# Kernel optimization log

Hardware: AMD Instinct MI355X
Metric: run time of the kernel (lower is better)

Reference implementation:

```python
import jax, jax.numpy as jnp
import numpy as np

K = 16          # number of nearest neighbors (kernel_size)
BN_EPS = 1e-5   # BatchNorm eps
LRELU_SLOPE = 0.2


def setup_inputs() -> dict:
    key = jax.random.key(0)
    k1, k2 = jax.random.split(key)
    B, C, N = 2, 64, 8192
    C_out = 64
    x = jax.random.normal(k1, (B, C, N, 1), dtype=jnp.float32)
    # Conv2d(in_channels*2, out_channels, kernel_size=1, bias=False)
    W = jax.random.normal(k2, (C_out, 2 * C), dtype=jnp.float32) * (1.0 / np.sqrt(2 * C))
    gamma = jnp.ones((C_out,), dtype=jnp.float32)
    beta = jnp.zeros((C_out,), dtype=jnp.float32)
    return {"x": x, "W": W, "gamma": gamma, "beta": beta}


def _knn_idx(f):
    """f: (B, C, N) point features. Returns nn_idx (B, N, K) of nearest neighbors
    (by squared euclidean distance, including self)."""
    pts = jnp.transpose(f, (0, 2, 1))                     # (B, N, C)
    sq = jnp.sum(pts * pts, axis=-1)                      # (B, N)
    inner = jnp.einsum('bnc,bmc->bnm', pts, pts)          # (B, N, N)
    dist = sq[:, :, None] - 2.0 * inner + sq[:, None, :]  # (B, N, N) squared dist
    # torch.topk(-pairwise_distance, k) -> indices of k smallest distances
    _, nn_idx = jax.lax.top_k(-dist, K)                   # (B, N, K)
    return nn_idx


def reference(x, W, gamma, beta):
    # x: (B, C, N, 1)
    f = x[:, :, :, 0]                                     # (B, C, N)
    nn_idx = _knn_idx(jax.lax.stop_gradient(f))           # (B, N, K), no grad (torch.no_grad)

    # EdgeConv features: x_i = center (broadcast), x_j = gathered neighbors
    x_j = jax.vmap(lambda fb, ib: fb[:, ib])(f, nn_idx)   # (B, C, N, K)
    x_i = f[:, :, :, None]                                # (B, C, N, 1) broadcasts over K
    feat = jnp.concatenate(
        [jnp.broadcast_to(x_i, x_j.shape), x_j - x_i], axis=1)  # (B, 2C, N, K)

    # 1x1 conv (no bias)
    y = jnp.einsum('oc,bcnk->bonk', W, feat)              # (B, C_out, N, K)

    # BatchNorm2d (training mode: batch statistics, biased variance)
    mean = jnp.mean(y, axis=(0, 2, 3), keepdims=True)
    var = jnp.mean(jnp.square(y - mean), axis=(0, 2, 3), keepdims=True)
    y = (y - mean) * jax.lax.rsqrt(var + BN_EPS)
    y = y * gamma[None, :, None, None] + beta[None, :, None, None]

    # LeakyReLU(0.2)
    y = jnp.where(y >= 0, y, LRELU_SLOPE * y)

    # max over neighbors
    return jnp.max(y, axis=-1)                            # (B, C_out, N)
```

## Files before the change

kernel.cpp:

```cpp
#include <hip/hip_runtime.h>
#include <hip/hip_bf16.h>

#define B 2
#define C 64
#define N 8192
#define K 16
#define CO 64
#define KSEG 4
#define NSTEP (N / KSEG / 64)

using s8v    = __attribute__((ext_vector_type(8)))  short;
using f32x16 = __attribute__((ext_vector_type(16))) float;

__device__ __forceinline__ unsigned short f2bf(float f) {
    unsigned u = __builtin_bit_cast(unsigned, f);
    u += 0x7fffu + ((u >> 16) & 1u);
    return (unsigned short)(u >> 16);
}
__device__ __forceinline__ float bf2f(unsigned short h) {
    unsigned u = ((unsigned)h) << 16;
    return __builtin_bit_cast(float, u);
}
__device__ __forceinline__ void gl_lds16(const void* g, void* l) {
    __builtin_amdgcn_global_load_lds((const __attribute__((address_space(1))) unsigned int*)g,
                                     (__attribute__((address_space(3))) unsigned int*)l, 16, 0, 0);
}

__global__ __launch_bounds__(256) void k_sqnorm(const float* __restrict__ f,
                                                float* __restrict__ sq) {
    int i = blockIdx.x * 256 + threadIdx.x;
    int b = i >> 13;
    int n = i & (N - 1);
    const float* fp = f + (size_t)b * C * N + n;
    float s = 0.f;
#pragma unroll
    for (int c = 0; c < C; ++c) {
        float v = fp[(size_t)c * N];
        s += v * v;
    }
    sq[i] = s;
}

__global__ __launch_bounds__(256) void k_prep(const float* __restrict__ x,
                                              unsigned short* __restrict__ Xh,
                                              unsigned short* __restrict__ Xm,
                                              unsigned short* __restrict__ Xl) {
    __shared__ float lt[64][65];
    int bid = blockIdx.x;
    int b = bid >> 7;
    int n0 = (bid & 127) * 64;
    int tid = threadIdx.x;
    int quarter = tid >> 6, j = tid & 63;
#pragma unroll
    for (int cc = 0; cc < 16; ++cc) {
        int c = quarter * 16 + cc;
        lt[c][j] = x[((size_t)b * C + c) * N + n0 + j];
    }
    __syncthreads();
#pragma unroll
    for (int cc = 0; cc < 16; ++cc) {
        int nl = quarter * 16 + cc;
        float v = lt[j][nl];
        unsigned short h = f2bf(v);
        float r1 = v - bf2f(h);
        unsigned short m = f2bf(r1);
        unsigned short l = f2bf(r1 - bf2f(m));
        size_t row = ((size_t)b * N + n0 + nl) * 64 + j;
        Xh[row] = h; Xm[row] = m; Xl[row] = l;
    }
}

__global__ __launch_bounds__(256, 2) void k_knn(
        const unsigned short* __restrict__ Xh,
        const unsigned short* __restrict__ Xm,
        const unsigned short* __restrict__ Xl,
        const float* __restrict__ sq,
        float* __restrict__ partd, int* __restrict__ parti) {
    __shared__ __align__(16) unsigned short lds[2][3][64 * 64];

    int bid = blockIdx.x;
    int seg = bid & 3;
    int qb  = (bid >> 2) & 63;
    int b   = bid >> 8;
    int tid = threadIdx.x;
    int w = tid >> 6, lane = tid & 63;
    int l31 = lane & 31, lhi = lane >> 5;
    int q = qb * 128 + w * 32 + l31;

    const unsigned short* Xs[3] = {Xh, Xm, Xl};

    s8v qf[3][4];
    {
        size_t qrow = ((size_t)b * N + q) * 64;
#pragma unroll
        for (int s = 0; s < 3; ++s)
#pragma unroll
            for (int kt = 0; kt < 4; ++kt)
                qf[s][kt] = *(const s8v*)&Xs[s][qrow + kt * 16 + lhi * 8];
    }

    float bd[16];
    int   bi16[16];
#pragma unroll
    for (int j = 0; j < 16; ++j) { bd[j] = -3.4e38f; bi16[j] = -1; }
    float worst = -3.4e38f;
    int wslot = 0;

    int segbase = seg * (N / KSEG);
    int srcRowOff = lane >> 3;
    int srcChunk  = (lane & 7) ^ (lane >> 3);

    {
        int cand0 = segbase;
#pragma unroll
        for (int jj = 0; jj < 6; ++jj) {
            int is = w * 6 + jj;
            int split = is >> 3, r0 = (is & 7) * 8;
            const unsigned short* gsrc = Xs[split] +
                ((size_t)(b * N + cand0 + r0 + srcRowOff)) * 64 + srcChunk * 8;
            gl_lds16(gsrc, &lds[0][split][r0 * 64]);
        }
    }

    for (int t = 0; t < NSTEP; ++t) {
        int cand0 = segbase + t * 64;
        int cb = t & 1;

        f32x16 acc[2];
#pragma unroll
        for (int ct = 0; ct < 2; ++ct) {
#pragma unroll
            for (int g = 0; g < 4; ++g) {
                float4 sv = *(const float4*)&sq[b * N + cand0 + ct * 32 + g * 8 + 4 * lhi];
                acc[ct][g * 4 + 0] = -0.5f * sv.x;
                acc[ct][g * 4 + 1] = -0.5f * sv.y;
                acc[ct][g * 4 + 2] = -0.5f * sv.z;
                acc[ct][g * 4 + 3] = -0.5f * sv.w;
            }
        }
        asm volatile("" ::: "memory");

        if (t + 1 < NSTEP) {
            int cn = cand0 + 64;
#pragma unroll
            for (int jj = 0; jj < 6; ++jj) {
                int is = w * 6 + jj;
                int split = is >> 3, r0 = (is & 7) * 8;
                const unsigned short* gsrc = Xs[split] +
                    ((size_t)(b * N + cn + r0 + srcRowOff)) * 64 + srcChunk * 8;
                gl_lds16(gsrc, &lds[cb ^ 1][split][r0 * 64]);
            }
            asm volatile("s_waitcnt vmcnt(6)" ::: "memory");
        } else {
            asm volatile("s_waitcnt vmcnt(0)" ::: "memory");
        }
        __syncthreads();

#pragma unroll
        for (int ct = 0; ct < 2; ++ct) {
            int arow = ct * 32 + l31;
            s8v af[3][4];
#pragma unroll
            for (int s = 0; s < 3; ++s)
#pragma unroll
                for (int kt = 0; kt < 4; ++kt)
                    af[s][kt] = *(const s8v*)&lds[cb][s][arow * 64 + (((kt * 2 + lhi) ^ (arow & 7)) * 8)];
            f32x16 a = acc[ct];
#pragma unroll
            for (int kt = 0; kt < 4; ++kt) {
                a = __builtin_amdgcn_mfma_f32_32x32x16_bf16(af[1][kt], qf[1][kt], a, 0, 0, 0);
                a = __builtin_amdgcn_mfma_f32_32x32x16_bf16(af[0][kt], qf[2][kt], a, 0, 0, 0);
                a = __builtin_amdgcn_mfma_f32_32x32x16_bf16(af[2][kt], qf[0][kt], a, 0, 0, 0);
                a = __builtin_amdgcn_mfma_f32_32x32x16_bf16(af[0][kt], qf[1][kt], a, 0, 0, 0);
                a = __builtin_amdgcn_mfma_f32_32x32x16_bf16(af[1][kt], qf[0][kt], a, 0, 0, 0);
                a = __builtin_amdgcn_mfma_f32_32x32x16_bf16(af[0][kt], qf[0][kt], a, 0, 0, 0);
            }
#pragma unroll
            for (int r = 0; r < 16; ++r) {
                float sc = a[r];
                if (sc > worst) {
                    int idx = cand0 + ct * 32 + (r & 3) + 8 * (r >> 2) + 4 * lhi;
#pragma unroll
                    for (int j = 0; j < 16; ++j)
                        if (j == wslot) { bd[j] = sc; bi16[j] = idx; }
                    worst = bd[0]; wslot = 0;
#pragma unroll
                    for (int j = 1; j < 16; ++j)
                        if (bd[j] < worst) { worst = bd[j]; wslot = j; }
                }
            }
        }
        __syncthreads();
    }

    int listid = seg * 2 + lhi;
    int bq = b * N + q;
#pragma unroll
    for (int j = 0; j < 16; ++j) {
        partd[(listid * 16 + j) * (B * N) + bq] = -bd[j];
        parti[(listid * 16 + j) * (B * N) + bq] = bi16[j];
    }
}

__global__ __launch_bounds__(256) void k_merge(const float* __restrict__ partd,
                                               const int* __restrict__ parti,
                                               int* __restrict__ nn) {
    int i = blockIdx.x * 256 + threadIdx.x;
    float bd[16];
    int   bi16[16];
#pragma unroll
    for (int j = 0; j < 16; ++j) { bd[j] = 3.4e38f; bi16[j] = -1; }
    float worst = 3.4e38f;
    int wslot = 0;
    for (int t = 0; t < 8 * 16; ++t) {
        float key = partd[t * (B * N) + i];
        int   idx = parti[t * (B * N) + i];
        if (key < worst) {
#pragma unroll
            for (int j = 0; j < 16; ++j)
                if (j == wslot) { bd[j] = key; bi16[j] = idx; }
            worst = bd[0]; wslot = 0;
#pragma unroll
            for (int j = 1; j < 16; ++j)
                if (bd[j] > worst) { worst = bd[j]; wslot = j; }
        }
    }
#pragma unroll
    for (int j = 0; j < 16; ++j) nn[i * 16 + j] = bi16[j];
}

__global__ __launch_bounds__(256) void k_ag(const float* __restrict__ f,
                                            const float* __restrict__ W,
                                            float* __restrict__ A,
                                            float* __restrict__ G) {
    __shared__ float lw[CO * 129];
    __shared__ float lf[C * 64];
    int bid = blockIdx.x;
    int b = bid >> 7;
    int n0 = (bid & 127) * 64;
    int tid = threadIdx.x;

    for (int idx = tid; idx < CO * 128; idx += 256) {
        int o = idx >> 7, c = idx & 127;
        lw[o * 129 + c] = W[idx];
    }
    for (int idx = tid; idx < C * 64; idx += 256) {
        int c = idx >> 6, nl = idx & 63;
        lf[idx] = f[(size_t)b * C * N + (size_t)c * N + n0 + nl];
    }
    __syncthreads();

    int o = tid & 63, qq = tid >> 6;
    for (int ii = 0; ii < 16; ++ii) {
        int nl = qq * 16 + ii;
        float fa = 0.f, fg = 0.f;
#pragma unroll
        for (int c = 0; c < C; ++c) {
            float fv = lf[c * 64 + nl];
            fa += lw[o * 129 + c] * fv;
            fg += lw[o * 129 + 64 + c] * fv;
        }
        int n = n0 + nl;
        A[((size_t)b * N + n) * 64 + o] = fa;
        G[((size_t)b * N + n) * 64 + o] = fg;
    }
}

__global__ __launch_bounds__(256) void k_stats(const float* __restrict__ A,
                                               const float* __restrict__ G,
                                               const int* __restrict__ nn,
                                               float* __restrict__ ymax,
                                               float* __restrict__ ymin,
                                               float* __restrict__ stats) {
    __shared__ int lidx[64 * K];
    __shared__ float red[256];
    int bid = blockIdx.x;
    int b = bid >> 7;
    int n0 = (bid & 127) * 64;
    int tid = threadIdx.x;

    for (int idx = tid; idx < 64 * K; idx += 256)
        lidx[idx] = nn[((size_t)b * N + n0) * K + idx];
    __syncthreads();

    int o = tid & 63, qq = tid >> 6;
    const float* Gb = G + (size_t)b * N * 64;
    float ssum = 0.f, ssq = 0.f;
    for (int ii = 0; ii < 16; ++ii) {
        int nl = qq * 16 + ii;
        int n = n0 + nl;
        float a = A[((size_t)b * N + n) * 64 + o];
        float g = Gb[(size_t)n * 64 + o];
        float d = a - g;
        float s1 = 0.f, s2 = 0.f;
        float gmx = -3.4e38f, gmn = 3.4e38f;
#pragma unroll
        for (int k = 0; k < K; ++k) {
            int j = lidx[nl * K + k];
            float gj = Gb[(size_t)j * 64 + o];
            s1 += gj;
            s2 += gj * gj;
            gmx = fmaxf(gmx, gj);
            gmn = fminf(gmn, gj);
        }
        ymax[((size_t)b * N + n) * 64 + o] = d + gmx;
        ymin[((size_t)b * N + n) * 64 + o] = d + gmn;
        ssum += (float)K * d + s1;
        ssq  += (float)K * d * d + 2.f * d * s1 + s2;
    }

    red[tid] = ssum; __syncthreads();
    if (qq == 0) {
        float t = red[o] + red[64 + o] + red[128 + o] + red[192 + o];
        atomicAdd(&stats[o], t);
    }
    __syncthreads();
    red[tid] = ssq; __syncthreads();
    if (qq == 0) {
        float t = red[o] + red[64 + o] + red[128 + o] + red[192 + o];
        atomicAdd(&stats[64 + o], t);
    }
}

__global__ __launch_bounds__(256) void k_final(const float* __restrict__ ymax,
                                               const float* __restrict__ ymin,
                                               const float* __restrict__ stats,
                                               const float* __restrict__ gamma,
                                               const float* __restrict__ beta,
                                               float* __restrict__ out) {
    __shared__ float lt[64 * 65];
    int bid = blockIdx.x;
    int b = bid >> 7;
    int n0 = (bid & 127) * 64;
    int tid = threadIdx.x;
    int o = tid & 63, qq = tid >> 6;

    const float Mcnt = (float)(B * N * K);
    float s1 = stats[o], s2 = stats[64 + o];
    float mean = s1 / Mcnt;
    float var = s2 / Mcnt - mean * mean;
    float inv = rsqrtf(var + 1e-5f);
    float scale = gamma[o] * inv;
    float shift = beta[o] - mean * scale;
    const float* src = (scale >= 0.f) ? ymax : ymin;

    for (int ii = 0; ii < 16; ++ii) {
        int nl = qq * 16 + ii;
        int n = n0 + nl;
        float v = src[((size_t)b * N + n) * 64 + o] * scale + shift;
        v = (v >= 0.f) ? v : 0.2f * v;
        lt[o * 65 + nl] = v;
    }
    __syncthreads();
    int nl2 = tid & 63;
    for (int ii = 0; ii < 16; ++ii) {
        int o2 = qq * 16 + ii;
        out[((size_t)b * CO + o2) * N + n0 + nl2] = lt[o2 * 65 + nl2];
    }
}

extern "C" void kernel_launch(void* const* d_in, const int* in_sizes, int n_in,
                              void* d_out, int out_size, void* d_ws, size_t ws_size,
                              hipStream_t stream) {
    const float* x     = (const float*)d_in[0];
    const float* W     = (const float*)d_in[1];
    const float* gamma = (const float*)d_in[2];
    const float* beta  = (const float*)d_in[3];
    float* out = (float*)d_out;

    char* ws = (char*)d_ws;
    float*          sq    = (float*)(ws + 0);
    float*          stats = (float*)(ws + 65536);
    int*            nn    = (int*)  (ws + 131072);
    float*          partd = (float*)(ws + 2228224);
    int*            parti = (int*)  (ws + 10616832);
    float*          A     = (float*)(ws + 2228224);
    float*          G     = (float*)(ws + 2228224 + 4194304);
    float*          ymax  = (float*)(ws + 10616832);
    float*          ymin  = (float*)(ws + 10616832 + 4194304);
    unsigned short* Xh    = (unsigned short*)(ws + 19005440);
    unsigned short* Xm    = (unsigned short*)(ws + 21102592);
    unsigned short* Xl    = (unsigned short*)(ws + 23199744);

    hipMemsetAsync(stats, 0, 512, stream);
    k_sqnorm<<<(B * N) / 256, 256, 0, stream>>>(x, sq);
    k_prep  <<<B * 128, 256, 0, stream>>>(x, Xh, Xm, Xl);
    k_knn   <<<B * 64 * KSEG, 256, 0, stream>>>(Xh, Xm, Xl, sq, partd, parti);
    k_merge <<<(B * N) / 256, 256, 0, stream>>>(partd, parti, nn);
    k_ag    <<<B * 128, 256, 0, stream>>>(x, W, A, G);
    k_stats <<<B * 128, 256, 0, stream>>>(A, G, nn, ymax, ymin, stats);
    k_final <<<B * 128, 256, 0, stream>>>(ymax, ymin, stats, gamma, beta, out);
}
```

Baseline: 575.3 us.

## Fuse sqnorm into prep and pack top-k slot ids into distance bits

Folds the squared-norm computation into the prep kernel, which now stores -0.5*|x|^2 directly, removing one kernel launch and one pass over x. In the KNN kernel, the per-thread top-16 list encodes the slot number in the low 4 mantissa bits of each score, so the worst entry and its slot come from a branch-free fminf tree instead of a compare-and-select scan. Neighbor indices move out of registers into an LDS array, which lowers register pressure but adds 16KB of LDS per block and a scattered LDS store on each insertion. Dropping the low 4 bits of the score slightly perturbs ordering among near-tied neighbors.

```diff
diff --git a/kernel.cpp b/kernel.cpp
--- a/kernel.cpp
+++ b/kernel.cpp
@@ -26,37 +26,30 @@
                                      (__attribute__((address_space(3))) unsigned int*)l, 16, 0, 0);
 }
 
-__global__ __launch_bounds__(256) void k_sqnorm(const float* __restrict__ f,
-                                                float* __restrict__ sq) {
-    int i = blockIdx.x * 256 + threadIdx.x;
-    int b = i >> 13;
-    int n = i & (N - 1);
-    const float* fp = f + (size_t)b * C * N + n;
-    float s = 0.f;
-#pragma unroll
-    for (int c = 0; c < C; ++c) {
-        float v = fp[(size_t)c * N];
-        s += v * v;
-    }
-    sq[i] = s;
-}
-
 __global__ __launch_bounds__(256) void k_prep(const float* __restrict__ x,
                                               unsigned short* __restrict__ Xh,
                                               unsigned short* __restrict__ Xm,
-                                              unsigned short* __restrict__ Xl) {
+                                              unsigned short* __restrict__ Xl,
+                                              float* __restrict__ nsq) {
     __shared__ float lt[64][65];
+    __shared__ float red[4 * 64];
     int bid = blockIdx.x;
     int b = bid >> 7;
     int n0 = (bid & 127) * 64;
     int tid = threadIdx.x;
     int quarter = tid >> 6, j = tid & 63;
+    float part = 0.f;
 #pragma unroll
     for (int cc = 0; cc < 16; ++cc) {
         int c = quarter * 16 + cc;
-        lt[c][j] = x[((size_t)b * C + c) * N + n0 + j];
-    }
-    __syncthreads();
+        float v = x[((size_t)b * C + c) * N + n0 + j];
+        lt[c][j] = v;
+        part += v * v;
+    }
+    red[quarter * 64 + j] = part;
+    __syncthreads();
+    if (quarter == 0)
+        nsq[b * N + n0 + j] = -0.5f * (red[j] + red[64 + j] + red[128 + j] + red[192 + j]);
 #pragma unroll
     for (int cc = 0; cc < 16; ++cc) {
         int nl = quarter * 16 + cc;
@@ -74,9 +67,10 @@
         const unsigned short* __restrict__ Xh,
         const unsigned short* __restrict__ Xm,
         const unsigned short* __restrict__ Xl,
-        const float* __restrict__ sq,
+        const float* __restrict__ nsq,
         float* __restrict__ partd, int* __restrict__ parti) {
     __shared__ __align__(16) unsigned short lds[2][3][64 * 64];
+    __shared__ int lidx[256 * 16];
 
     int bid = blockIdx.x;
     int seg = bid & 3;
@@ -100,11 +94,11 @@
     }
 
     float bd[16];
-    int   bi16[16];
-#pragma unroll
-    for (int j = 0; j < 16; ++j) { bd[j] = -3.4e38f; bi16[j] = -1; }
-    float worst = -3.4e38f;
-    int wslot = 0;
+#pragma unroll
+    for (int j = 0; j < 16; ++j)
+        bd[j] = __builtin_bit_cast(float, 0xFF7FFFF0u | (unsigned)j);
+    float wmin = __builtin_bit_cast(float, 0xFF7FFFFFu);
+    int wslot = 15;
 
     int segbase = seg * (N / KSEG);
     int srcRowOff = lane >> 3;
@@ -131,11 +125,11 @@
         for (int ct = 0; ct < 2; ++ct) {
 #pragma unroll
             for (int g = 0; g < 4; ++g) {
-                float4 sv = *(const float4*)&sq[b * N + cand0 + ct * 32 + g * 8 + 4 * lhi];
-                acc[ct][g * 4 + 0] = -0.5f * sv.x;
-                acc[ct][g * 4 + 1] = -0.5f * sv.y;
-                acc[ct][g * 4 + 2] = -0.5f * sv.z;
-                acc[ct][g * 4 + 3] = -0.5f * sv.w;
+                float4 sv = *(const float4*)&nsq[b * N + cand0 + ct * 32 + g * 8 + 4 * lhi];
+                acc[ct][g * 4 + 0] = sv.x;
+                acc[ct][g * 4 + 1] = sv.y;
+                acc[ct][g * 4 + 2] = sv.z;
+                acc[ct][g * 4 + 3] = sv.w;
             }
         }
         asm volatile("" ::: "memory");
@@ -178,15 +172,19 @@
 #pragma unroll
             for (int r = 0; r < 16; ++r) {
                 float sc = a[r];
-                if (sc > worst) {
+                if (sc > wmin) {
                     int idx = cand0 + ct * 32 + (r & 3) + 8 * (r >> 2) + 4 * lhi;
+                    unsigned pv = __builtin_bit_cast(unsigned, sc) & ~15u;
 #pragma unroll
                     for (int j = 0; j < 16; ++j)
-                        if (j == wslot) { bd[j] = sc; bi16[j] = idx; }
-                    worst = bd[0]; wslot = 0;
-#pragma unroll
-                    for (int j = 1; j < 16; ++j)
-                        if (bd[j] < worst) { worst = bd[j]; wslot = j; }
+                        if (wslot == j) bd[j] = __builtin_bit_cast(float, pv | (unsigned)j);
+                    lidx[(tid << 4) | wslot] = idx;
+                    float m0 = fminf(fminf(bd[0],  bd[1]),  fminf(bd[2],  bd[3]));
+                    float m1 = fminf(fminf(bd[4],  bd[5]),  fminf(bd[6],  bd[7]));
+                    float m2 = fminf(fminf(bd[8],  bd[9]),  fminf(bd[10], bd[11]));
+                    float m3 = fminf(fminf(bd[12], bd[13]), fminf(bd[14], bd[15]));
+                    wmin = fminf(fminf(m0, m1), fminf(m2, m3));
+                    wslot = (int)(__builtin_bit_cast(unsigned, wmin) & 15u);
                 }
             }
         }
@@ -195,10 +193,11 @@
 
     int listid = seg * 2 + lhi;
     int bq = b * N + q;
+    int base = tid << 4;
 #pragma unroll
     for (int j = 0; j < 16; ++j) {
         partd[(listid * 16 + j) * (B * N) + bq] = -bd[j];
-        parti[(listid * 16 + j) * (B * N) + bq] = bi16[j];
+        parti[(listid * 16 + j) * (B * N) + bq] = lidx[base + j];
     }
 }
 
@@ -369,7 +368,7 @@
     float* out = (float*)d_out;
 
     char* ws = (char*)d_ws;
-    float*          sq    = (float*)(ws + 0);
+    float*          nsq   = (float*)(ws + 0);
     float*          stats = (float*)(ws + 65536);
     int*            nn    = (int*)  (ws + 131072);
     float*          partd = (float*)(ws + 2228224);
@@ -383,9 +382,8 @@
     unsigned short* Xl    = (unsigned short*)(ws + 23199744);
 
     hipMemsetAsync(stats, 0, 512, stream);
-    k_sqnorm<<<(B * N) / 256, 256, 0, stream>>>(x, sq);
-    k_prep  <<<B * 128, 256, 0, stream>>>(x, Xh, Xm, Xl);
-    k_knn   <<<B * 64 * KSEG, 256, 0, stream>>>(Xh, Xm, Xl, sq, partd, parti);
+    k_prep  <<<B * 128, 256, 0, stream>>>(x, Xh, Xm, Xl, nsq);
+    k_knn   <<<B * 64 * KSEG, 256, 0, stream>>>(Xh, Xm, Xl, nsq, partd, parti);
     k_merge <<<(B * N) / 256, 256, 0, stream>>>(partd, parti, nn);
     k_ag    <<<B * 128, 256, 0, stream>>>(x, W, A, G);
     k_stats <<<B * 128, 256, 0, stream>>>(A, G, nn, ymax, ymin, stats);
```

Measured after the change: 489.0 us. 1.18x faster.
